# Kernel tuning notes

Hardware: AMD Instinct MI355X
Metric: run time of the kernel (lower is better)

The kernel has to match this reference:

```python
import jax, jax.numpy as jnp
import numpy as np

NUM_HEADS = 16
ROPE_BASE = 10000.0
MAX_POS = 4096


def _rope_tables(head_dim):
    inv_freq = 1.0 / (ROPE_BASE ** (np.arange(0, head_dim, 2, dtype=np.float32) / head_dim))
    freqs = np.arange(MAX_POS, dtype=np.float32)[:, None] * inv_freq[None, :]
    emb = np.concatenate([freqs, freqs], axis=-1)  # [MAX_POS, head_dim]
    return jnp.asarray(np.cos(emb)), jnp.asarray(np.sin(emb))


def _rotate_half(x):
    d = x.shape[-1] // 2
    return jnp.concatenate([-x[..., d:], x[..., :d]], axis=-1)


def _apply_rope(x, pos, cos_t, sin_t):
    # x: [B,H,S,D], pos: [B,S]
    cos = cos_t[pos][:, None]  # [B,1,S,D]
    sin = sin_t[pos][:, None]
    return x * cos + _rotate_half(x) * sin


def setup_inputs() -> dict:
    key = jax.random.key(0)
    ks = jax.random.split(key, 8)
    B, N, M, C = 2, 2048, 2048, 1024
    s = 1.0 / np.sqrt(C)
    return {
        "query": jax.random.normal(ks[0], (B, N, C), jnp.float32),
        "key": jax.random.normal(ks[1], (B, M, C), jnp.float32),
        "query_pos": jnp.broadcast_to(jnp.arange(N, dtype=jnp.int32), (B, N)),
        "key_pos": jnp.broadcast_to(jnp.arange(M, dtype=jnp.int32), (B, M)),
        "Wq": jax.random.normal(ks[2], (C, C), jnp.float32) * s,
        "bq": jnp.zeros((C,), jnp.float32),
        "Wk": jax.random.normal(ks[3], (C, C), jnp.float32) * s,
        "Wv": jax.random.normal(ks[4], (C, C), jnp.float32) * s,
        "bv": jnp.zeros((C,), jnp.float32),
        "Wo": jax.random.normal(ks[5], (C, C), jnp.float32) * s,
        "bo": jnp.zeros((C,), jnp.float32),
    }


def reference(query, key, query_pos, key_pos, Wq, bq, Wk, Wv, bv, Wo, bo):
    B, N, C = query.shape
    M = key.shape[1]
    H = NUM_HEADS
    D = C // H
    scale = D ** -0.5
    cos_t, sin_t = _rope_tables(D)

    value = key  # value defaults to key
    identity = query

    q = (query @ Wq.T + bq).reshape(B, N, H, D).transpose(0, 2, 1, 3)
    k = (key @ Wk.T).reshape(B, M, H, D).transpose(0, 2, 1, 3)
    v = (value @ Wv.T + bv).reshape(B, M, H, D).transpose(0, 2, 1, 3)

    q = _apply_rope(q, query_pos, cos_t, sin_t)
    k = _apply_rope(k, key_pos, cos_t, sin_t)

    attn = jnp.einsum('bhnd,bhmd->bhnm', q, k) * scale
    attn = jax.nn.softmax(attn, axis=-1)
    x = jnp.einsum('bhnm,bhmd->bhnd', attn, v)  # [B,H,N,D]
    x = x.transpose(0, 2, 1, 3).reshape(B, N, C)
    x = x @ Wo.T + bo
    return x + identity
```

## Files before the change

### kernel.cpp

```cpp
#include <hip/hip_runtime.h>
#include <hip/hip_bf16.h>
#include <stdint.h>

#define B_ 2
#define N_ 2048
#define M_ 2048
#define C_ 1024
#define H_ 16
#define D_ 64

typedef __attribute__((ext_vector_type(8))) short s16x8;
typedef __attribute__((ext_vector_type(4))) short s16x4;
typedef __attribute__((ext_vector_type(4))) float f32x4;
typedef __attribute__((ext_vector_type(16))) float f32x16;

__device__ __attribute__((always_inline)) inline short f2b(float f){
    __hip_bfloat16 h = __float2bfloat16(f); short s; __builtin_memcpy(&s, &h, 2); return s;
}
__device__ __attribute__((always_inline)) inline float b2f(short s){
    __hip_bfloat16 h; __builtin_memcpy(&h, &s, 2); return __bfloat162float(h);
}

#define MFMA16(a,b,c) __builtin_amdgcn_mfma_f32_16x16x32_bf16(a,b,c,0,0,0)
#define MFMA32(a,b,c) __builtin_amdgcn_mfma_f32_32x32x16_bf16(a,b,c,0,0,0)

__device__ __attribute__((always_inline)) inline void gl_lds16(const void* g, void* l){
    __builtin_amdgcn_global_load_lds((__attribute__((address_space(1))) void*)g,
                                     (__attribute__((address_space(3))) void*)l, 16, 0, 0);
}
__device__ __attribute__((always_inline)) inline unsigned cvtpk(float lo, float hi){
    unsigned r;
    asm("v_cvt_pk_bf16_f32 %0, %1, %2" : "=v"(r) : "v"(lo), "v"(hi));
    return r;
}
__device__ __attribute__((always_inline)) inline void lane32swap(unsigned &a, unsigned &b){
    asm("v_permlane32_swap_b32 %0, %1" : "+v"(a), "+v"(b));
}

__global__ void cvt_all(const float* __restrict__ q, const float* __restrict__ k,
                        const float* __restrict__ wq, const float* __restrict__ wk,
                        const float* __restrict__ wv, const float* __restrict__ wo,
                        short* __restrict__ dst){
    long i = ((long)blockIdx.x * 256 + threadIdx.x) * 8;
    const float* src; long off;
    if      (i <  4194304L){ src = q;  off = i; }
    else if (i <  8388608L){ src = k;  off = i - 4194304L; }
    else if (i <  9437184L){ src = wq; off = i - 8388608L; }
    else if (i < 10485760L){ src = wk; off = i - 9437184L; }
    else if (i < 11534336L){ src = wv; off = i - 10485760L; }
    else                   { src = wo; off = i - 11534336L; }
    float4 a = *(const float4*)(src + off);
    float4 b = *(const float4*)(src + off + 4);
    s16x8 o;
    o[0]=f2b(a.x); o[1]=f2b(a.y); o[2]=f2b(a.z); o[3]=f2b(a.w);
    o[4]=f2b(b.x); o[5]=f2b(b.y); o[6]=f2b(b.z); o[7]=f2b(b.w);
    *(s16x8*)(dst + i) = o;
}

__global__ __launch_bounds__(256, 3) void gemm_qkv(
    const short* __restrict__ qbf, const short* __restrict__ kbf,
    const short* __restrict__ W,
    const float* __restrict__ bq, const float* __restrict__ bv,
    const int* __restrict__ kpos,
    short* __restrict__ qproj, short* __restrict__ kproj, short* __restrict__ vT)
{
    __shared__ short sb[8704];
    short* As = sb;
    short* Bs = sb + 4096;
    const int n0 = blockIdx.x * 128, m0 = blockIdx.y * 128;
    const int sel = n0 >> 10;
    const short* A = (sel == 0) ? qbf : kbf;
    const int tid = threadIdx.x, lane = tid & 63, wave = tid >> 6;
    const int quad = lane >> 4, l16 = lane & 15;
    const int wr = (wave >> 1) * 64, wc = (wave & 1) * 64;
    const int srow = lane >> 2, scol = (lane & 3) * 8;

    f32x4 acc[4][4] = {};

    const short* Ag = A + (size_t)(m0 + wave * 32 + srow) * C_ + scol;
    const short* Bg = W + (size_t)(n0 + wave * 32 + srow) * C_ + scol;
    short* lA0 = As + (wave * 32) * 32;
    short* lA1 = As + (wave * 32 + 16) * 32;
    short* lB0 = Bs + (wave * 32) * 32;
    short* lB1 = Bs + (wave * 32 + 16) * 32;

    for (int k0 = 0; k0 < C_; k0 += 32){
        __syncthreads();
        gl_lds16(Ag + k0, lA0);
        gl_lds16(Ag + k0 + 16 * (size_t)C_, lA1);
        gl_lds16(Bg + k0, lB0);
        gl_lds16(Bg + k0 + 16 * (size_t)C_, lB1);
        __syncthreads();
        s16x8 af[4], bfr[4];
        #pragma unroll
        for (int t = 0; t < 4; t++) af[t]  = *(const s16x8*)&As[(wr + t*16 + l16) * 32 + quad * 8];
        #pragma unroll
        for (int t = 0; t < 4; t++) bfr[t] = *(const s16x8*)&Bs[(wc + t*16 + l16) * 32 + quad * 8];
        #pragma unroll
        for (int i = 0; i < 4; i++)
            #pragma unroll
            for (int j = 0; j < 4; j++)
                acc[i][j] = MFMA16(af[i], bfr[j], acc[i][j]);
    }

    if (sel == 0){
        #pragma unroll
        for (int j = 0; j < 4; j++){
            int c = n0 + wc + j * 16 + l16;
            float bb = bq[c];
            #pragma unroll
            for (int i = 0; i < 4; i++){
                int row = m0 + wr + i * 16 + quad * 4;
                #pragma unroll
                for (int r = 0; r < 4; r++)
                    qproj[(size_t)(row + r) * C_ + c] = f2b(acc[i][j][r] + bb);
            }
        }
    } else if (sel == 1){
        #pragma unroll
        for (int j2 = 0; j2 < 2; j2++){
            int c1 = n0 - 1024 + wc + j2 * 16 + l16;
            int irot = c1 & 63;
            float invf = exp2f((float)irot * (-13.287712379549449f / 32.0f));
            #pragma unroll
            for (int i = 0; i < 4; i++){
                int row = m0 + wr + i * 16 + quad * 4;
                #pragma unroll
                for (int r = 0; r < 4; r++){
                    float pos = (float)kpos[row + r];
                    float ang = pos * invf;
                    float cs = __cosf(ang), sn = __sinf(ang);
                    float x1 = acc[i][j2][r], x2 = acc[i][j2 + 2][r];
                    kproj[(size_t)(row + r) * C_ + c1]      = f2b(x1 * cs - x2 * sn);
                    kproj[(size_t)(row + r) * C_ + c1 + 32] = f2b(x2 * cs + x1 * sn);
                }
            }
        }
    } else {
        short* Vt = sb;
        const int bat = m0 >> 11;
        const int mbase = m0 & 2047;
        #pragma unroll
        for (int p = 0; p < 2; p++){
            __syncthreads();
            if ((wave & 1) == p){
                #pragma unroll
                for (int j = 0; j < 4; j++){
                    int c_local = j * 16 + l16;
                    float bb = bv[n0 - 2048 + p * 64 + c_local];
                    #pragma unroll
                    for (int i = 0; i < 4; i++){
                        int row = wr + i * 16 + quad * 4;
                        unsigned u0 = (unsigned)(unsigned short)f2b(acc[i][j][0] + bb) |
                                      ((unsigned)(unsigned short)f2b(acc[i][j][1] + bb) << 16);
                        unsigned u1 = (unsigned)(unsigned short)f2b(acc[i][j][2] + bb) |
                                      ((unsigned)(unsigned short)f2b(acc[i][j][3] + bb) << 16);
                        uint2 u; u.x = u0; u.y = u1;
                        *(uint2*)&Vt[c_local * 136 + row] = u;
                    }
                }
            }
            __syncthreads();
            #pragma unroll
            for (int it = 0; it < 4; it++){
                int qq = it * 256 + tid;
                int c_local = qq >> 4, mm = (qq & 15) * 8;
                int colg = n0 - 2048 + p * 64 + c_local;
                int hh = colg >> 6, dd = colg & 63;
                s16x8 v = *(const s16x8*)&Vt[c_local * 136 + mm];
                *(s16x8*)&vT[(((size_t)(bat * H_ + hh)) * D_ + dd) * M_ + mbase + mm] = v;
            }
        }
    }
}

__global__ __launch_bounds__(256, 4) void gemm_out(
    const short* __restrict__ A, const short* __restrict__ W,
    const float* __restrict__ bias, const float* __restrict__ resid,
    float* __restrict__ outf)
{
    __shared__ short As[128 * 32];
    __shared__ short Bs[64 * 32];
    const int n0 = blockIdx.x * 64, m0 = blockIdx.y * 128;
    const int tid = threadIdx.x, lane = tid & 63, wave = tid >> 6;
    const int quad = lane >> 4, l16 = lane & 15;
    const int srow = lane >> 2, scol = (lane & 3) * 8;

    f32x4 acc[2][4] = {};
    const short* Ag = A + (size_t)(m0 + wave * 32 + srow) * C_ + scol;
    const short* Bg = W + (size_t)(n0 + wave * 16 + srow) * C_ + scol;
    short* lA0 = As + (wave * 32) * 32;
    short* lA1 = As + (wave * 32 + 16) * 32;
    short* lB  = Bs + (wave * 16) * 32;

    for (int k0 = 0; k0 < C_; k0 += 32){
        __syncthreads();
        gl_lds16(Ag + k0, lA0);
        gl_lds16(Ag + k0 + 16 * (size_t)C_, lA1);
        gl_lds16(Bg + k0, lB);
        __syncthreads();
        s16x8 af[2], bfr[4];
        #pragma unroll
        for (int t = 0; t < 2; t++) af[t]  = *(const s16x8*)&As[(wave*32 + t*16 + l16) * 32 + quad * 8];
        #pragma unroll
        for (int t = 0; t < 4; t++) bfr[t] = *(const s16x8*)&Bs[(t*16 + l16) * 32 + quad * 8];
        #pragma unroll
        for (int i = 0; i < 2; i++)
            #pragma unroll
            for (int j = 0; j < 4; j++)
                acc[i][j] = MFMA16(af[i], bfr[j], acc[i][j]);
    }

    #pragma unroll
    for (int j = 0; j < 4; j++){
        int c = n0 + j * 16 + l16;
        float bb = bias[c];
        #pragma unroll
        for (int i = 0; i < 2; i++){
            int row = m0 + wave * 32 + i * 16 + quad * 4;
            #pragma unroll
            for (int r = 0; r < 4; r++){
                size_t idx = (size_t)(row + r) * C_ + c;
                outf[idx] = acc[i][j][r] + bb + resid[idx];
            }
        }
    }
}

#define QK_STEP(ST, SV) do {                                                          \
    const short* Kp_ = &smem[((ST) & 3) * 4352];                                      \
    s16x4 kfa_[4][2];                                                                 \
    _Pragma("unroll")                                                                 \
    for (int c = 0; c < 4; c++){                                                      \
        const short* a_ = &Kp_[(kq * 32 + l32) * 68 + c * 16 + hi * 8];               \
        kfa_[c][0] = *(const s16x4*)a_; kfa_[c][1] = *(const s16x4*)(a_ + 4);         \
    }                                                                                 \
    _Pragma("unroll")                                                                 \
    for (int qt = 0; qt < 2; qt++){                                                   \
        f32x16 sv0_ = {};                                                             \
        _Pragma("unroll")                                                             \
        for (int c = 0; c < 4; c++){                                                  \
            s16x8 ka_ = __builtin_shufflevector(kfa_[c][0], kfa_[c][1],               \
                                                0,1,2,3,4,5,6,7);                     \
            sv0_ = MFMA32(ka_, qf[qt][c], sv0_);                                      \
        }                                                                             \
        SV[qt] = sv0_;                                                                \
    }                                                                                 \
} while(0)

#define FINISH_STEP(ST, SV) do {                                                      \
    const short* Vp_ = &smem[17408 + ((ST) & 3) * 4352];                              \
    s16x8 vfa_[2][2];                                                                 \
    _Pragma("unroll")                                                                 \
    for (int dt = 0; dt < 2; dt++)                                                    \
        _Pragma("unroll")                                                             \
        for (int c = 0; c < 2; c++){                                                  \
            const short* a_ = &Vp_[(dt * 32 + l32) * 68 + kq * 32 + c * 16 + hi * 8]; \
            vfa_[dt][c] = __builtin_shufflevector(*(const s16x4*)a_,                  \
                                                  *(const s16x4*)(a_ + 4),            \
                                                  0,1,2,3,4,5,6,7);                   \
        }                                                                             \
    s16x8 pfa_[2][2];                                                                 \
    _Pragma("unroll")                                                                 \
    for (int qt = 0; qt < 2; qt++){                                                   \
        _Pragma("unroll")                                                             \
        for (int e = 0; e < 16; e++) SV[qt][e] = __builtin_amdgcn_exp2f(SV[qt][e]);   \
        float ls_ = 0.f;                                                              \
        _Pragma("unroll")                                                             \
        for (int e = 0; e < 16; e += 4)                                               \
            ls_ += (SV[qt][e] + SV[qt][e+1]) + (SV[qt][e+2] + SV[qt][e+3]);           \
        lacc[qt] += ls_;                                                              \
        _Pragma("unroll")                                                             \
        for (int c = 0; c < 2; c++){                                                  \
            unsigned a1_ = cvtpk(SV[qt][8*c + 0], SV[qt][8*c + 1]);                   \
            unsigned a2_ = cvtpk(SV[qt][8*c + 2], SV[qt][8*c + 3]);                   \
            unsigned b1_ = cvtpk(SV[qt][8*c + 4], SV[qt][8*c + 5]);                   \
            unsigned b2_ = cvtpk(SV[qt][8*c + 6], SV[qt][8*c + 7]);                   \
            lane32swap(a1_, b1_);                                                     \
            lane32swap(a2_, b2_);                                                     \
            union { unsigned u[4]; s16x8 v; } pk_;                                    \
            pk_.u[0] = a1_; pk_.u[1] = a2_; pk_.u[2] = b1_; pk_.u[3] = b2_;           \
            pfa_[qt][c] = pk_.v;                                                      \
        }                                                                             \
    }                                                                                 \
    _Pragma("unroll")                                                                 \
    for (int qt = 0; qt < 2; qt++)                                                    \
        _Pragma("unroll")                                                             \
        for (int dt = 0; dt < 2; dt++)                                                \
            _Pragma("unroll")                                                         \
            for (int c = 0; c < 2; c++)                                               \
                oacc[qt][dt] = MFMA32(pfa_[qt][c], vfa_[dt][c], oacc[qt][dt]);        \
} while(0)

#define STAGE_STEP(ST) do {                                                           \
    if ((ST) < 31){                                                                   \
        int bn_ = ((ST) + 1) & 3;                                                     \
        _Pragma("unroll")                                                             \
        for (int ii = 0; ii < 2; ii++){                                               \
            int row_ = srow0 + 32 * ii;                                               \
            short* kd_ = &smem[bn_ * 4352 + row_ * 68 + sseg];                        \
            *(uint2*)kd_ = kreg[ii].u[0]; *(uint2*)(kd_ + 4) = kreg[ii].u[1];         \
            short* vd_ = &smem[17408 + bn_ * 4352 + row_ * 68 + sseg];                \
            *(uint2*)vd_ = vreg[ii].u[0]; *(uint2*)(vd_ + 4) = vreg[ii].u[1];         \
        }                                                                             \
    }                                                                                 \
    if ((ST) < 30){                                                                   \
        _Pragma("unroll")                                                             \
        for (int ii = 0; ii < 2; ii++){                                               \
            int row_ = srow0 + 32 * ii;                                               \
            kreg[ii].v = *(const s16x8*)&kg[((size_t)(((ST) + 2) * 64 + row_)) * C_ + sseg]; \
            vreg[ii].v = *(const s16x8*)&vg[(size_t)row_ * M_ + ((ST) + 2) * 64 + sseg];     \
        }                                                                             \
    }                                                                                 \
    asm volatile("s_waitcnt lgkmcnt(0)" ::: "memory");                                \
    __builtin_amdgcn_s_barrier();                                                     \
} while(0)

__global__ __launch_bounds__(256, 2) void flash_attn(
    const short* __restrict__ q, const short* __restrict__ k,
    const short* __restrict__ vt, short* __restrict__ o,
    const int* __restrict__ qpos)
{
    __shared__ short smem[35328];
    const int b = blockIdx.y >> 4, h = blockIdx.y & 15;
    const int n0 = blockIdx.x * 128;
    const int tid = threadIdx.x, lane = tid & 63, wave = tid >> 6;
    const int hi = lane >> 5, l32 = lane & 31;
    const int wq = wave & 1, kq = wave >> 1;

    s16x8 qf[2][4];
    const float fac = 0.18033688011112042f;
    #pragma unroll
    for (int qt = 0; qt < 2; qt++){
        int qrow = n0 + wq * 64 + qt * 32 + l32;
        const short* qg = &q[((size_t)(b * N_ + qrow)) * C_ + h * D_];
        float pos = (float)qpos[b * N_ + qrow];
        s16x8 raw[4];
        #pragma unroll
        for (int c = 0; c < 4; c++) raw[c] = *(const s16x8*)&qg[c * 16 + hi * 8];
        #pragma unroll
        for (int c = 0; c < 2; c++){
            s16x8 olo, ohi8;
            #pragma unroll
            for (int j = 0; j < 8; j++){
                int irot = c * 16 + hi * 8 + j;
                float invf = exp2f((float)irot * (-13.287712379549449f / 32.0f));
                float ang = pos * invf;
                float cs = __cosf(ang), sn = __sinf(ang);
                float x1 = b2f(raw[c][j]), x2 = b2f(raw[c + 2][j]);
                olo[j]  = f2b((x1 * cs - x2 * sn) * fac);
                ohi8[j] = f2b((x2 * cs + x1 * sn) * fac);
            }
            qf[qt][c] = olo; qf[qt][c + 2] = ohi8;
        }
    }

    const short* kg = k  + (size_t)(b * M_) * C_ + h * D_;
    const short* vg = vt + ((size_t)(b * H_ + h)) * D_ * M_;
    const int srow0 = tid >> 3, sseg = (tid & 7) * 8;

    union V8 { s16x8 v; uint2 u[2]; };
    V8 kreg[2], vreg[2];

    #pragma unroll
    for (int ii = 0; ii < 2; ii++){
        int row = srow0 + 32 * ii;
        kreg[ii].v = *(const s16x8*)&kg[(size_t)row * C_ + sseg];
        vreg[ii].v = *(const s16x8*)&vg[(size_t)row * M_ + sseg];
    }
    #pragma unroll
    for (int ii = 0; ii < 2; ii++){
        int row = srow0 + 32 * ii;
        short* kd = &smem[row * 68 + sseg];
        *(uint2*)kd = kreg[ii].u[0]; *(uint2*)(kd + 4) = kreg[ii].u[1];
        short* vd = &smem[17408 + row * 68 + sseg];
        *(uint2*)vd = vreg[ii].u[0]; *(uint2*)(vd + 4) = vreg[ii].u[1];
    }
    #pragma unroll
    for (int ii = 0; ii < 2; ii++){
        int row = srow0 + 32 * ii;
        kreg[ii].v = *(const s16x8*)&kg[(size_t)(64 + row) * C_ + sseg];
        vreg[ii].v = *(const s16x8*)&vg[(size_t)row * M_ + 64 + sseg];
    }
    asm volatile("s_waitcnt lgkmcnt(0)" ::: "memory");
    __builtin_amdgcn_s_barrier();

    f32x16 zero16 = {};
    f32x16 oacc[2][2] = {zero16, zero16, zero16, zero16};
    float lacc[2] = {0.f, 0.f};

    f32x16 svA[2], svB[2];

    QK_STEP(0, svA);
    STAGE_STEP(0);
    for (int st = 1; st <= 29; st += 2){
        QK_STEP(st, svB);
        FINISH_STEP(st - 1, svA);
        STAGE_STEP(st);
        QK_STEP(st + 1, svA);
        FINISH_STEP(st, svB);
        STAGE_STEP(st + 1);
    }
    QK_STEP(31, svB);
    FINISH_STEP(30, svA);
    FINISH_STEP(31, svB);

    __syncthreads();

    float* LO   = (float*)smem;
    float* Lsum = (float*)&smem[34816];
    float* Linv = Lsum + 128;

    float l0[2];
    #pragma unroll
    for (int qt = 0; qt < 2; qt++)
        l0[qt] = lacc[qt] + __shfl_xor(lacc[qt], 32);

    if (kq == 1){
        #pragma unroll
        for (int qt = 0; qt < 2; qt++)
            Lsum[wq * 64 + qt * 32 + l32] = l0[qt];
        #pragma unroll
        for (int qt = 0; qt < 2; qt++)
            #pragma unroll
            for (int dt = 0; dt < 2; dt++)
                #pragma unroll
                for (int e = 0; e < 16; e++){
                    int qrow = wq * 64 + qt * 32 + (e & 3) + 8 * (e >> 2) + 4 * hi;
                    LO[qrow * 65 + dt * 32 + l32] = oacc[qt][dt][e];
                }
    }
    __syncthreads();
    if (kq == 0){
        #pragma unroll
        for (int qt = 0; qt < 2; qt++){
            float lt = l0[qt] + Lsum[wq * 64 + qt * 32 + l32];
            Linv[wq * 64 + qt * 32 + l32] = 1.0f / lt;
        }
        asm volatile("s_waitcnt lgkmcnt(0)" ::: "memory");
        #pragma unroll
        for (int qt = 0; qt < 2; qt++)
            #pragma unroll
            for (int dt = 0; dt < 2; dt++)
                #pragma unroll
                for (int e = 0; e < 16; e++){
                    int qrow = wq * 64 + qt * 32 + (e & 3) + 8 * (e >> 2) + 4 * hi;
                    float val = (oacc[qt][dt][e] + LO[qrow * 65 + dt * 32 + l32]) * Linv[qrow];
                    o[((size_t)(b * N_ + n0 + qrow)) * C_ + h * D_ + dt * 32 + l32] = f2b(val);
                }
    }
}

extern "C" void kernel_launch(void* const* d_in, const int* in_sizes, int n_in,
                              void* d_out, int out_size, void* d_ws, size_t ws_size,
                              hipStream_t stream) {
    const float* query = (const float*)d_in[0];
    const float* key   = (const float*)d_in[1];
    const int*   qpos  = (const int*)d_in[2];
    const int*   kpos  = (const int*)d_in[3];
    const float* Wq    = (const float*)d_in[4];
    const float* bq    = (const float*)d_in[5];
    const float* Wk    = (const float*)d_in[6];
    const float* Wv    = (const float*)d_in[7];
    const float* bv    = (const float*)d_in[8];
    const float* Wo    = (const float*)d_in[9];
    const float* bo    = (const float*)d_in[10];
    float* out = (float*)d_out;

    const size_t E4M = (size_t)4 * 1024 * 1024;
    const size_t E1M = (size_t)1024 * 1024;
    short* ws    = (short*)d_ws;
    short* qbf   = ws;
    short* kbf   = qbf   + E4M;
    short* wqkvb = kbf   + E4M;
    short* wob   = wqkvb + 3 * E1M;
    short* qproj = wob   + E1M;
    short* kproj = qproj + E4M;
    short* vT    = kproj + E4M;
    short* attn  = qbf;

    cvt_all<<<6144, 256, 0, stream>>>(query, key, Wq, Wk, Wv, Wo, ws);

    gemm_qkv<<<dim3(24, 32), 256, 0, stream>>>(qbf, kbf, wqkvb, bq, bv, kpos,
                                               qproj, kproj, vT);

    flash_attn<<<dim3(16, 32), 256, 0, stream>>>(qproj, kproj, vT, attn, qpos);

    gemm_out<<<dim3(16, 32), 256, 0, stream>>>(attn, wob, bo, query, out);
}
```

Before: 211.7 us.

## Process KV tiles in pairs per barrier and remap attention blocks across XCDs

The flash attention main loop drops the software-pipelined QK/finish split, where the QK MFMA of one tile overlapped the softmax and PV of the previous tile. It now computes two full tiles per iteration from a 2x2 LDS buffer ring, with double register staging of global loads, so only one barrier runs per pair of tiles instead of one per tile. The grid also becomes 1D with a block-id swizzle, so consecutive blocks landing on the same XCD share the same batch/head and reuse K/V in L2. In exchange, MFMA/exp overlap inside each tile is lost and more registers are held for the staged loads.

```diff
diff --git a/kernel.cpp b/kernel.cpp
--- a/kernel.cpp
+++ b/kernel.cpp
@@ -227,60 +227,53 @@
     }
 }
 
-#define QK_STEP(ST, SV) do {                                                          \
-    const short* Kp_ = &smem[((ST) & 3) * 4352];                                      \
-    s16x4 kfa_[4][2];                                                                 \
+#define COMPUTE_TILE(BI) do {                                                         \
+    const short* Kp_ = &smem[(BI) * 4352];                                            \
+    const short* Vp_ = &smem[17408 + (BI) * 4352];                                    \
+    s16x4 kf_[4][2];                                                                  \
     _Pragma("unroll")                                                                 \
     for (int c = 0; c < 4; c++){                                                      \
         const short* a_ = &Kp_[(kq * 32 + l32) * 68 + c * 16 + hi * 8];               \
-        kfa_[c][0] = *(const s16x4*)a_; kfa_[c][1] = *(const s16x4*)(a_ + 4);         \
+        kf_[c][0] = *(const s16x4*)a_; kf_[c][1] = *(const s16x4*)(a_ + 4);           \
     }                                                                                 \
-    _Pragma("unroll")                                                                 \
-    for (int qt = 0; qt < 2; qt++){                                                   \
-        f32x16 sv0_ = {};                                                             \
-        _Pragma("unroll")                                                             \
-        for (int c = 0; c < 4; c++){                                                  \
-            s16x8 ka_ = __builtin_shufflevector(kfa_[c][0], kfa_[c][1],               \
-                                                0,1,2,3,4,5,6,7);                     \
-            sv0_ = MFMA32(ka_, qf[qt][c], sv0_);                                      \
-        }                                                                             \
-        SV[qt] = sv0_;                                                                \
-    }                                                                                 \
-} while(0)
-
-#define FINISH_STEP(ST, SV) do {                                                      \
-    const short* Vp_ = &smem[17408 + ((ST) & 3) * 4352];                              \
-    s16x8 vfa_[2][2];                                                                 \
+    s16x8 vf_[2][2];                                                                  \
     _Pragma("unroll")                                                                 \
     for (int dt = 0; dt < 2; dt++)                                                    \
         _Pragma("unroll")                                                             \
         for (int c = 0; c < 2; c++){                                                  \
             const short* a_ = &Vp_[(dt * 32 + l32) * 68 + kq * 32 + c * 16 + hi * 8]; \
-            vfa_[dt][c] = __builtin_shufflevector(*(const s16x4*)a_,                  \
-                                                  *(const s16x4*)(a_ + 4),            \
-                                                  0,1,2,3,4,5,6,7);                   \
+            vf_[dt][c] = __builtin_shufflevector(*(const s16x4*)a_,                   \
+                                                 *(const s16x4*)(a_ + 4),             \
+                                                 0,1,2,3,4,5,6,7);                    \
         }                                                                             \
-    s16x8 pfa_[2][2];                                                                 \
+    s16x8 pf_[2][2];                                                                  \
     _Pragma("unroll")                                                                 \
     for (int qt = 0; qt < 2; qt++){                                                   \
-        _Pragma("unroll")                                                             \
-        for (int e = 0; e < 16; e++) SV[qt][e] = __builtin_amdgcn_exp2f(SV[qt][e]);   \
+        f32x16 sv_ = {};                                                              \
+        _Pragma("unroll")                                                             \
+        for (int c = 0; c < 4; c++){                                                  \
+            s16x8 ka_ = __builtin_shufflevector(kf_[c][0], kf_[c][1],                 \
+                                                0,1,2,3,4,5,6,7);                     \
+            sv_ = MFMA32(ka_, qf[qt][c], sv_);                                        \
+        }                                                                             \
+        float pe_[16];                                                                \
+        _Pragma("unroll")                                                             \
+        for (int e = 0; e < 16; e++) pe_[e] = __builtin_amdgcn_exp2f(sv_[e]);         \
         float ls_ = 0.f;                                                              \
         _Pragma("unroll")                                                             \
-        for (int e = 0; e < 16; e += 4)                                               \
-            ls_ += (SV[qt][e] + SV[qt][e+1]) + (SV[qt][e+2] + SV[qt][e+3]);           \
+        for (int e = 0; e < 16; e += 4) ls_ += (pe_[e]+pe_[e+1]) + (pe_[e+2]+pe_[e+3]);\
         lacc[qt] += ls_;                                                              \
         _Pragma("unroll")                                                             \
         for (int c = 0; c < 2; c++){                                                  \
-            unsigned a1_ = cvtpk(SV[qt][8*c + 0], SV[qt][8*c + 1]);                   \
-            unsigned a2_ = cvtpk(SV[qt][8*c + 2], SV[qt][8*c + 3]);                   \
-            unsigned b1_ = cvtpk(SV[qt][8*c + 4], SV[qt][8*c + 5]);                   \
-            unsigned b2_ = cvtpk(SV[qt][8*c + 6], SV[qt][8*c + 7]);                   \
+            unsigned a1_ = cvtpk(pe_[8*c + 0], pe_[8*c + 1]);                         \
+            unsigned a2_ = cvtpk(pe_[8*c + 2], pe_[8*c + 3]);                         \
+            unsigned b1_ = cvtpk(pe_[8*c + 4], pe_[8*c + 5]);                         \
+            unsigned b2_ = cvtpk(pe_[8*c + 6], pe_[8*c + 7]);                         \
             lane32swap(a1_, b1_);                                                     \
             lane32swap(a2_, b2_);                                                     \
             union { unsigned u[4]; s16x8 v; } pk_;                                    \
             pk_.u[0] = a1_; pk_.u[1] = a2_; pk_.u[2] = b1_; pk_.u[3] = b2_;           \
-            pfa_[qt][c] = pk_.v;                                                      \
+            pf_[qt][c] = pk_.v;                                                       \
         }                                                                             \
     }                                                                                 \
     _Pragma("unroll")                                                                 \
@@ -289,31 +282,27 @@
         for (int dt = 0; dt < 2; dt++)                                                \
             _Pragma("unroll")                                                         \
             for (int c = 0; c < 2; c++)                                               \
-                oacc[qt][dt] = MFMA32(pfa_[qt][c], vfa_[dt][c], oacc[qt][dt]);        \
+                oacc[qt][dt] = MFMA32(pf_[qt][c], vf_[dt][c], oacc[qt][dt]);          \
 } while(0)
 
-#define STAGE_STEP(ST) do {                                                           \
-    if ((ST) < 31){                                                                   \
-        int bn_ = ((ST) + 1) & 3;                                                     \
-        _Pragma("unroll")                                                             \
-        for (int ii = 0; ii < 2; ii++){                                               \
-            int row_ = srow0 + 32 * ii;                                               \
-            short* kd_ = &smem[bn_ * 4352 + row_ * 68 + sseg];                        \
-            *(uint2*)kd_ = kreg[ii].u[0]; *(uint2*)(kd_ + 4) = kreg[ii].u[1];         \
-            short* vd_ = &smem[17408 + bn_ * 4352 + row_ * 68 + sseg];                \
-            *(uint2*)vd_ = vreg[ii].u[0]; *(uint2*)(vd_ + 4) = vreg[ii].u[1];         \
-        }                                                                             \
+#define WRITE_SET(BUF, KR, VR) do {                                                   \
+    _Pragma("unroll")                                                                 \
+    for (int ii = 0; ii < 2; ii++){                                                   \
+        int row_ = srow0 + 32 * ii;                                                   \
+        short* kd_ = &smem[(BUF) * 4352 + row_ * 68 + sseg];                          \
+        *(uint2*)kd_ = KR[ii].u[0]; *(uint2*)(kd_ + 4) = KR[ii].u[1];                 \
+        short* vd_ = &smem[17408 + (BUF) * 4352 + row_ * 68 + sseg];                  \
+        *(uint2*)vd_ = VR[ii].u[0]; *(uint2*)(vd_ + 4) = VR[ii].u[1];                 \
     }                                                                                 \
-    if ((ST) < 30){                                                                   \
-        _Pragma("unroll")                                                             \
-        for (int ii = 0; ii < 2; ii++){                                               \
-            int row_ = srow0 + 32 * ii;                                               \
-            kreg[ii].v = *(const s16x8*)&kg[((size_t)(((ST) + 2) * 64 + row_)) * C_ + sseg]; \
-            vreg[ii].v = *(const s16x8*)&vg[(size_t)row_ * M_ + ((ST) + 2) * 64 + sseg];     \
-        }                                                                             \
+} while(0)
+
+#define LOAD_SET(KR, VR, T) do {                                                      \
+    _Pragma("unroll")                                                                 \
+    for (int ii = 0; ii < 2; ii++){                                                   \
+        int row_ = srow0 + 32 * ii;                                                   \
+        KR[ii].v = *(const s16x8*)&kg[((size_t)((T) * 64 + row_)) * C_ + sseg];       \
+        VR[ii].v = *(const s16x8*)&vg[(size_t)row_ * M_ + (T) * 64 + sseg];           \
     }                                                                                 \
-    asm volatile("s_waitcnt lgkmcnt(0)" ::: "memory");                                \
-    __builtin_amdgcn_s_barrier();                                                     \
 } while(0)
 
 __global__ __launch_bounds__(256, 2) void flash_attn(
@@ -322,8 +311,11 @@
     const int* __restrict__ qpos)
 {
     __shared__ short smem[35328];
-    const int b = blockIdx.y >> 4, h = blockIdx.y & 15;
-    const int n0 = blockIdx.x * 128;
+    const int bid = blockIdx.x;
+    const int wgid = (bid & 7) * 64 + (bid >> 3);
+    const int y = wgid >> 4;
+    const int n0 = (wgid & 15) * 128;
+    const int b = y >> 4, h = y & 15;
     const int tid = threadIdx.x, lane = tid & 63, wave = tid >> 6;
     const int hi = lane >> 5, l32 = lane & 31;
     const int wq = wave & 1, kq = wave >> 1;
@@ -360,28 +352,14 @@
     const int srow0 = tid >> 3, sseg = (tid & 7) * 8;
 
     union V8 { s16x8 v; uint2 u[2]; };
-    V8 kreg[2], vreg[2];
-
-    #pragma unroll
-    for (int ii = 0; ii < 2; ii++){
-        int row = srow0 + 32 * ii;
-        kreg[ii].v = *(const s16x8*)&kg[(size_t)row * C_ + sseg];
-        vreg[ii].v = *(const s16x8*)&vg[(size_t)row * M_ + sseg];
-    }
-    #pragma unroll
-    for (int ii = 0; ii < 2; ii++){
-        int row = srow0 + 32 * ii;
-        short* kd = &smem[row * 68 + sseg];
-        *(uint2*)kd = kreg[ii].u[0]; *(uint2*)(kd + 4) = kreg[ii].u[1];
-        short* vd = &smem[17408 + row * 68 + sseg];
-        *(uint2*)vd = vreg[ii].u[0]; *(uint2*)(vd + 4) = vreg[ii].u[1];
-    }
-    #pragma unroll
-    for (int ii = 0; ii < 2; ii++){
-        int row = srow0 + 32 * ii;
-        kreg[ii].v = *(const s16x8*)&kg[(size_t)(64 + row) * C_ + sseg];
-        vreg[ii].v = *(const s16x8*)&vg[(size_t)row * M_ + 64 + sseg];
-    }
+    V8 kregA[2], vregA[2], kregB[2], vregB[2];
+
+    LOAD_SET(kregA, vregA, 0);
+    LOAD_SET(kregB, vregB, 1);
+    WRITE_SET(0, kregA, vregA);
+    WRITE_SET(1, kregB, vregB);
+    LOAD_SET(kregA, vregA, 2);
+    LOAD_SET(kregB, vregB, 3);
     asm volatile("s_waitcnt lgkmcnt(0)" ::: "memory");
     __builtin_amdgcn_s_barrier();
 
@@ -389,21 +367,19 @@
     f32x16 oacc[2][2] = {zero16, zero16, zero16, zero16};
     float lacc[2] = {0.f, 0.f};
 
-    f32x16 svA[2], svB[2];
-
-    QK_STEP(0, svA);
-    STAGE_STEP(0);
-    for (int st = 1; st <= 29; st += 2){
-        QK_STEP(st, svB);
-        FINISH_STEP(st - 1, svA);
-        STAGE_STEP(st);
-        QK_STEP(st + 1, svA);
-        FINISH_STEP(st, svB);
-        STAGE_STEP(st + 1);
-    }
-    QK_STEP(31, svB);
-    FINISH_STEP(30, svA);
-    FINISH_STEP(31, svB);
+    for (int iv = 0; iv < 16; iv++){
+        const int p = (iv & 1) << 1;
+        COMPUTE_TILE(p);
+        if (iv < 15) WRITE_SET(p ^ 2, kregA, vregA);
+        COMPUTE_TILE(p + 1);
+        if (iv < 15) WRITE_SET((p ^ 2) + 1, kregB, vregB);
+        if (iv < 14){
+            LOAD_SET(kregA, vregA, 2 * iv + 4);
+            LOAD_SET(kregB, vregB, 2 * iv + 5);
+        }
+        asm volatile("s_waitcnt lgkmcnt(0)" ::: "memory");
+        __builtin_amdgcn_s_barrier();
+    }
 
     __syncthreads();
 
@@ -484,7 +460,7 @@
     gemm_qkv<<<dim3(24, 32), 256, 0, stream>>>(qbf, kbf, wqkvb, bq, bv, kpos,
                                                qproj, kproj, vT);
 
-    flash_attn<<<dim3(16, 32), 256, 0, stream>>>(qproj, kproj, vT, attn, qpos);
+    flash_attn<<<512, 256, 0, stream>>>(qproj, kproj, vT, attn, qpos);
 
     gemm_out<<<dim3(16, 32), 256, 0, stream>>>(attn, wob, bo, query, out);
 }
```

After: 209.1 us. About the same (-1.2%).
